# Performance work log

Measured on AMD Instinct MI355X. Metric: run time of the kernel, lower is better.

## Reference

```python
import jax, jax.numpy as jnp
import numpy as np

B, L, H = 8, 4096, 768  # batch, max_length, attn_size (hidden)


def setup_inputs() -> dict:
    key = jax.random.key(0)
    ks = jax.random.split(key, 8)
    s = 1.0 / np.sqrt(H)  # nn.Linear default init scale (uniform bound)
    x = jax.random.normal(ks[0], (B, L, H), dtype=jnp.float32)
    Wq = jax.random.uniform(ks[1], (H, H), jnp.float32, -s, s)
    bq = jax.random.uniform(ks[2], (H,), jnp.float32, -s, s)
    Wk = jax.random.uniform(ks[3], (H, H), jnp.float32, -s, s)
    bk = jax.random.uniform(ks[4], (H,), jnp.float32, -s, s)
    Wv = jax.random.uniform(ks[5], (H, H), jnp.float32, -s, s)
    bv = jax.random.uniform(ks[6], (H,), jnp.float32, -s, s)
    gamma = jnp.zeros((1,), dtype=jnp.float32)  # nn.Parameter(torch.zeros(1))
    return {"x": x, "Wq": Wq, "bq": bq, "Wk": Wk, "bk": bk,
            "Wv": Wv, "bv": bv, "gamma": gamma}


def reference(x, Wq, bq, Wk, bk, Wv, bv, gamma):
    # Linear projections: y = x @ W^T + b   (torch nn.Linear convention)
    q = jnp.einsum('bld,ed->ble', x, Wq) + bq  # (B, L, H)
    k = jnp.einsum('bld,ed->ble', x, Wk) + bk
    v = jnp.einsum('bld,ed->ble', x, Wv) + bv
    # energy = bmm(Q^T, K): contracts over sequence -> (B, H, H)
    energy = jnp.einsum('bld,ble->bde', q, k)
    attention = jax.nn.softmax(energy, axis=-1)  # (B, H, H), softmax over last hidden dim
    # out = bmm(V, attention^T): out[b,l,i] = sum_j V[b,l,j] * A[b,i,j]
    out = jnp.einsum('blj,bij->bli', v, attention)
    # neg_out uses (1 - A); since sum_j V[b,l,j]*(1-A[b,i,j]) = rowsum(V) - out,
    # we fuse instead of materializing a second bmm over (1 - A).
    neg_out = jnp.sum(v, axis=-1, keepdims=True) - out
    g = gamma[0]
    return (g * out + x, g * neg_out + x)
```

## Files before the change

kernel.cpp:

```cpp
#include <hip/hip_runtime.h>
#include <hip/hip_bf16.h>


#define HD 768
#define LSEQ 4096
#define BATCH 8
#define LDSS 40

typedef unsigned short u16;
typedef __attribute__((ext_vector_type(8))) short frag_ab;
typedef __attribute__((ext_vector_type(4))) float f32x4;

struct alignas(8) U16x4 { u16 x, y, z, w; };

__device__ inline u16 f2bf(float f) {
  union { float f; unsigned u; } v; v.f = f;
  unsigned u = v.u;
  u += 0x7FFFu + ((u >> 16) & 1u);
  return (u16)(u >> 16);
}


template <typename T>
__device__ inline void stage_tile(u16* lds, const T* src, int ld, int tid) {
#pragma unroll
  for (int i = 0; i < 4; ++i) {
    int idx = tid + 256 * i;
    int r = idx >> 3;
    int kv = (idx & 7) * 4;
    if constexpr (sizeof(T) == 4) {
      float4 v = *(const float4*)(src + (size_t)r * ld + kv);
      U16x4 h;
      h.x = f2bf(v.x); h.y = f2bf(v.y); h.z = f2bf(v.z); h.w = f2bf(v.w);
      *(U16x4*)(lds + r * LDSS + kv) = h;
    } else {
      *(U16x4*)(lds + r * LDSS + kv) = *(const U16x4*)(src + (size_t)r * ld + kv);
    }
  }
}

template <typename TP, typename TQ>
__device__ inline void gemm_core(const TP* Pt, const TQ* Qt, int ldp, int ldq, int K,
                                 u16* ldsA, u16* ldsB, f32x4 (&acc)[4][4]) {
  const int tid = threadIdx.x;
  const int lane = tid & 63;
  const int wm = tid >> 7, wn = (tid >> 6) & 1;
  for (int kk = 0; kk < K; kk += 32) {
    stage_tile(ldsA, Pt + kk, ldp, tid);
    stage_tile(ldsB, Qt + kk, ldq, tid);
    __syncthreads();
    const u16* bA = ldsA + (wm * 64 + (lane & 15)) * LDSS + 8 * (lane >> 4);
    const u16* bB = ldsB + (wn * 64 + (lane & 15)) * LDSS + 8 * (lane >> 4);
    frag_ab a[4], b[4];
#pragma unroll
    for (int i = 0; i < 4; ++i) a[i] = *(const frag_ab*)(bA + i * 16 * LDSS);
#pragma unroll
    for (int j = 0; j < 4; ++j) b[j] = *(const frag_ab*)(bB + j * 16 * LDSS);
#pragma unroll
    for (int i = 0; i < 4; ++i)
#pragma unroll
      for (int j = 0; j < 4; ++j)
        acc[i][j] = __builtin_amdgcn_mfma_f32_16x16x32_bf16(a[i], b[j], acc[i][j], 0, 0, 0);
    __syncthreads();
  }
}

template <typename TP, typename TQ>
__global__ __launch_bounds__(256) void k_gemm(const TP* __restrict__ P, const TQ* __restrict__ Q,
                                              float* __restrict__ C, int ldp, int ldq, int ldc,
                                              int K, int tilesM, int tilesN, long sP, long sQ,
                                              long sC) {
  __shared__ u16 ldsA[128 * LDSS];
  __shared__ u16 ldsB[128 * LDSS];
  int bid = blockIdx.x;
  int tn = bid % tilesN;
  int tm = (bid / tilesN) % tilesM;
  int b = bid / (tilesN * tilesM);
  const TP* Pt = P + b * sP + (long)(tm * 128) * ldp;
  const TQ* Qt = Q + b * sQ + (long)(tn * 128) * ldq;
  f32x4 acc[4][4] = {};
  gemm_core(Pt, Qt, ldp, ldq, K, ldsA, ldsB, acc);
  const int lane = threadIdx.x & 63;
  const int wm = threadIdx.x >> 7, wn = (threadIdx.x >> 6) & 1;
  float* Cb = C + b * sC;
#pragma unroll
  for (int i = 0; i < 4; ++i)
#pragma unroll
    for (int j = 0; j < 4; ++j)
#pragma unroll
      for (int r = 0; r < 4; ++r) {
        int row = tm * 128 + wm * 64 + i * 16 + 4 * (lane >> 4) + r;
        int col = tn * 128 + wn * 64 + j * 16 + (lane & 15);
        Cb[(long)row * ldc + col] = acc[i][j][r];
      }
}

__global__ __launch_bounds__(256) void k_gemm_bias(const float* __restrict__ P,
                                                   const float* __restrict__ Q,
                                                   float* __restrict__ C, long sP, long sC,
                                                   const float* __restrict__ bq,
                                                   const float* __restrict__ bk,
                                                   const float* __restrict__ qb,
                                                   const float* __restrict__ kbp) {
  __shared__ u16 ldsA[128 * LDSS];
  __shared__ u16 ldsB[128 * LDSS];
  int bid = blockIdx.x;
  int tn = bid % 6;
  int tm = (bid / 6) % 6;
  int b = bid / 36;
  const float* Pt = P + b * sP + (long)(tm * 128) * HD;
  const float* Qt = Q + (long)(tn * 128) * HD;
  f32x4 acc[4][4] = {};
  gemm_core(Pt, Qt, HD, HD, HD, ldsA, ldsB, acc);
  const int lane = threadIdx.x & 63;
  const int wm = threadIdx.x >> 7, wn = (threadIdx.x >> 6) & 1;
  float* Cb = C + b * sC;
  const float* qbb = qb + b * HD;
  const float* kbb = kbp + b * HD;
#pragma unroll
  for (int i = 0; i < 4; ++i)
#pragma unroll
    for (int j = 0; j < 4; ++j)
#pragma unroll
      for (int r = 0; r < 4; ++r) {
        int row = tm * 128 + wm * 64 + i * 16 + 4 * (lane >> 4) + r;
        int col = tn * 128 + wn * 64 + j * 16 + (lane & 15);
        Cb[(long)row * HD + col] = acc[i][j][r] + bq[row] * kbb[col] + bk[col] * qbb[row];
      }
}

__global__ __launch_bounds__(256) void k_final(const float* __restrict__ x,
                                               const float* __restrict__ Mw,
                                               const float* __restrict__ cvec,
                                               const float* __restrict__ rsv,
                                               const float* __restrict__ bvs,
                                               const float* __restrict__ gamma,
                                               float* __restrict__ out) {
  __shared__ u16 ldsA[128 * LDSS];
  __shared__ u16 ldsB[128 * LDSS];
  int bid = blockIdx.x;
  int tn = bid % 6;
  int tm = (bid / 6) % 32;
  int b = bid / 192;
  const float* Pt = x + ((long)b * LSEQ + tm * 128) * HD;
  const float* Qt = Mw + (long)b * HD * HD + (long)(tn * 128) * HD;
  f32x4 acc[4][4] = {};
  gemm_core(Pt, Qt, HD, HD, HD, ldsA, ldsB, acc);
  const int lane = threadIdx.x & 63;
  const int wm = threadIdx.x >> 7, wn = (threadIdx.x >> 6) & 1;
  const float g = gamma[0];
  const float bvsum = bvs[0];
  const float* cb = cvec + b * HD;
  const float* rb = rsv + b * LSEQ;
  float* out2 = out + (long)BATCH * LSEQ * HD;
#pragma unroll
  for (int i = 0; i < 4; ++i)
#pragma unroll
    for (int j = 0; j < 4; ++j)
#pragma unroll
      for (int r = 0; r < 4; ++r) {
        int row = tm * 128 + wm * 64 + i * 16 + 4 * (lane >> 4) + r;
        int col = tn * 128 + wn * 64 + j * 16 + (lane & 15);
        float o = acc[i][j][r] + cb[col];
        long gi = ((long)b * LSEQ + row) * HD + col;
        float xv = x[gi];
        out[gi] = g * o + xv;
        out2[gi] = g * ((rb[row] + bvsum) - o) + xv;
      }
}


__global__ __launch_bounds__(256) void k_trans(const float* __restrict__ x, u16* __restrict__ Xt,
                                               float* __restrict__ s, float* __restrict__ rsv,
                                               const float* __restrict__ wvsum) {
  __shared__ float tile[64][65];
  __shared__ float red[4][64];
  int bid = blockIdx.x;
  int ft = bid % 12;
  int lt = (bid / 12) % 64;
  int b = bid / 768;
  int l0 = lt * 64, f0 = ft * 64;
  const float* xb = x + ((long)b * LSEQ + l0) * HD + f0;
  int t = threadIdx.x;
  int fi = t & 63, tg = t >> 6;
  float csum = 0.f;
#pragma unroll
  for (int i = 0; i < 16; ++i) {
    int li = tg * 16 + i;
    float v = xb[(long)li * HD + fi];
    tile[li][fi] = v;
    csum += v;
  }
  red[tg][fi] = csum;
  __syncthreads();
  if (tg == 0) atomicAdd(&s[b * HD + f0 + fi], red[0][fi] + red[1][fi] + red[2][fi] + red[3][fi]);
  int li2 = t & 63, fg = t >> 6;
  float rsum = 0.f;
  u16* Xtb = Xt + ((long)b * HD + f0) * LSEQ + l0;
#pragma unroll
  for (int i = 0; i < 16; ++i) {
    int fi2 = fg * 16 + i;
    float v = tile[li2][fi2];
    rsum += v * wvsum[f0 + fi2];
    Xtb[(long)fi2 * LSEQ + li2] = f2bf(v);
  }
  __syncthreads();
  red[fg][li2] = rsum;
  __syncthreads();
  if (fg == 0)
    atomicAdd(&rsv[b * LSEQ + l0 + li2], red[0][li2] + red[1][li2] + red[2][li2] + red[3][li2]);
}

__global__ __launch_bounds__(256) void k_wv(const float* __restrict__ Wv, u16* __restrict__ WvT,
                                            float* __restrict__ wvsum) {
  __shared__ float red[256];
  long idx = (long)blockIdx.x * 256 + threadIdx.x;
  int f = (int)(idx / HD);
  int j = (int)(idx % HD);
  float v = Wv[(long)j * HD + f];
  WvT[(long)f * HD + j] = f2bf(v);
  red[threadIdx.x] = v;
  __syncthreads();
  for (int off = 128; off > 0; off >>= 1) {
    if (threadIdx.x < off) red[threadIdx.x] += red[threadIdx.x + off];
    __syncthreads();
  }
  if (threadIdx.x == 0) atomicAdd(&wvsum[f], red[0]);
}

__global__ __launch_bounds__(256) void k_bvsum(const float* __restrict__ bv,
                                               float* __restrict__ bvs) {
  __shared__ float red[256];
  int t = threadIdx.x;
  red[t] = bv[t] + bv[t + 256] + bv[t + 512];
  __syncthreads();
  for (int off = 128; off > 0; off >>= 1) {
    if (t < off) red[t] += red[t + off];
    __syncthreads();
  }
  if (t == 0) bvs[0] = red[0];
}

__global__ __launch_bounds__(256) void k_qbkb(const float* __restrict__ Wq,
                                              const float* __restrict__ Wk,
                                              const float* __restrict__ bk,
                                              const float* __restrict__ s, float* __restrict__ qb,
                                              float* __restrict__ kbp) {
  __shared__ float ss[HD];
  int idx = blockIdx.x * 256 + threadIdx.x;
  int b = idx / (2 * HD);
  int rem = idx % (2 * HD);
  int mat = rem / HD;
  int d = rem % HD;
  const float* sb = s + b * HD;
  ss[threadIdx.x] = sb[threadIdx.x];
  ss[threadIdx.x + 256] = sb[threadIdx.x + 256];
  ss[threadIdx.x + 512] = sb[threadIdx.x + 512];
  __syncthreads();
  const float* Wr = (mat ? Wk : Wq) + (long)d * HD;
  float acc = 0.f;
  for (int f2 = 0; f2 < HD; ++f2) acc += ss[f2] * Wr[f2];
  if (mat)
    kbp[b * HD + d] = acc + (float)LSEQ * bk[d];
  else
    qb[b * HD + d] = acc;
}

__device__ inline float block_red(float v, int op, float* sm) {
#pragma unroll
  for (int o = 32; o > 0; o >>= 1) {
    float w = __shfl_xor(v, o);
    v = op ? (v + w) : fmaxf(v, w);
  }
  int wid = threadIdx.x >> 6;
  if ((threadIdx.x & 63) == 0) sm[wid] = v;
  __syncthreads();
  float r = op ? (sm[0] + sm[1] + sm[2] + sm[3])
              : fmaxf(fmaxf(sm[0], sm[1]), fmaxf(sm[2], sm[3]));
  __syncthreads();
  return r;
}

__global__ __launch_bounds__(256) void k_softmax(float* __restrict__ A,
                                                 const float* __restrict__ bv,
                                                 float* __restrict__ cvec) {
  __shared__ float sm[4];
  long ridx = blockIdx.x;
  float* Ar = A + ridx * HD;
  int t = threadIdx.x;
  float v0 = Ar[t], v1 = Ar[t + 256], v2 = Ar[t + 512];
  float mx = block_red(fmaxf(fmaxf(v0, v1), v2), 0, sm);
  v0 = __expf(v0 - mx);
  v1 = __expf(v1 - mx);
  v2 = __expf(v2 - mx);
  float sum = block_red(v0 + v1 + v2, 1, sm);
  float inv = 1.0f / sum;
  v0 *= inv; v1 *= inv; v2 *= inv;
  Ar[t] = v0; Ar[t + 256] = v1; Ar[t + 512] = v2;
  float cp = v0 * bv[t] + v1 * bv[t + 256] + v2 * bv[t + 512];
  cp = block_red(cp, 1, sm);
  if (t == 0) cvec[ridx] = cp;
}

extern "C" void kernel_launch(void* const* d_in, const int* in_sizes, int n_in, void* d_out,
                              int out_size, void* d_ws, size_t ws_size, hipStream_t stream) {
  const float* x = (const float*)d_in[0];
  const float* Wq = (const float*)d_in[1];
  const float* bq = (const float*)d_in[2];
  const float* Wk = (const float*)d_in[3];
  const float* bk = (const float*)d_in[4];
  const float* Wv = (const float*)d_in[5];
  const float* bv = (const float*)d_in[6];
  const float* gamma = (const float*)d_in[7];
  float* out = (float*)d_out;

  float* ws = (float*)d_ws;
  float* s = ws;
  float* rsv = s + BATCH * HD;
  float* wvsum = rsv + BATCH * LSEQ;
  float* bvs = wvsum + HD;
  float* qb = bvs + 4;
  float* kbp = qb + BATCH * HD;
  float* cvec = kbp + BATCH * HD;
  u16* WvT = (u16*)(cvec + BATCH * HD);
  float* Mw = (float*)(WvT + HD * HD);

  u16* Xt = (u16*)d_out;
  float* G = (float*)d_out + 12582912;
  float* V1 = G + (long)BATCH * HD * HD;
  float* Abuf = V1 + (long)BATCH * HD * HD;

  size_t zbytes = (size_t)(BATCH * HD + BATCH * LSEQ + HD + 4) * sizeof(float);
  hipMemsetAsync(d_ws, 0, zbytes, stream);

  k_wv<<<2304, 256, 0, stream>>>(Wv, WvT, wvsum);
  k_bvsum<<<1, 256, 0, stream>>>(bv, bvs);
  k_trans<<<BATCH * 64 * 12, 256, 0, stream>>>(x, Xt, s, rsv, wvsum);
  k_gemm<u16, u16><<<BATCH * 36, 256, 0, stream>>>(Xt, Xt, G, LSEQ, LSEQ, HD, LSEQ, 6, 6,
                                                   (long)HD * LSEQ, (long)HD * LSEQ,
                                                   (long)HD * HD);
  k_qbkb<<<48, 256, 0, stream>>>(Wq, Wk, bk, s, qb, kbp);
  k_gemm<float, float><<<BATCH * 36, 256, 0, stream>>>(Wq, G, V1, HD, HD, HD, HD, 6, 6, 0L,
                                                       (long)HD * HD, (long)HD * HD);
  k_gemm_bias<<<BATCH * 36, 256, 0, stream>>>(V1, Wk, Abuf, (long)HD * HD, (long)HD * HD, bq, bk,
                                              qb, kbp);
  k_softmax<<<BATCH * HD, 256, 0, stream>>>(Abuf, bv, cvec);
  k_gemm<float, u16><<<BATCH * 36, 256, 0, stream>>>(Abuf, WvT, Mw, HD, HD, HD, HD, 6, 6,
                                                     (long)HD * HD, 0L, (long)HD * HD);
  k_final<<<BATCH * 32 * 6, 256, 0, stream>>>(x, Mw, cvec, rsv, bvs, gamma, out);
}
```

Before: 729.1 us.

## Stage bf16 intermediates and use direct global-to-LDS loads in GEMMs

Converts intermediate matrices (Gram, V1, attention, Mw) and the weights Wq/Wk to bf16 up front, so every GEMM operand except fp32 inputs is staged with async global_load_lds instead of per-thread load-convert-store. When workspace allows, the transpose kernel also writes a bf16 copy of x so the final GEMM reads half the bytes. LDS padding is dropped to fit the direct-load layout, which may introduce bank conflicts. The qb/kb dot product is also vectorised.

```diff
diff --git a/kernel.cpp b/kernel.cpp
--- a/kernel.cpp
+++ b/kernel.cpp
@@ -5,11 +5,12 @@
 #define HD 768
 #define LSEQ 4096
 #define BATCH 8
-#define LDSS 40
 
 typedef unsigned short u16;
 typedef __attribute__((ext_vector_type(8))) short frag_ab;
 typedef __attribute__((ext_vector_type(4))) float f32x4;
+#define AS1 __attribute__((address_space(1)))
+#define AS3 __attribute__((address_space(3)))
 
 struct alignas(8) U16x4 { u16 x, y, z, w; };
 
@@ -21,41 +22,51 @@
 }
 
 
-template <typename T>
-__device__ inline void stage_tile(u16* lds, const T* src, int ld, int tid) {
+__device__ inline void stage_g2l(u16* lds, const u16* src, int ld, int tid) {
+  int w = tid >> 6, l = tid & 63;
+  int r0 = w * 32 + (l >> 2);
+  int kc = (l & 3) * 8;
+  const u16* g0 = src + (size_t)r0 * ld + kc;
+  const u16* g1 = g0 + (size_t)16 * ld;
+  u16* l0 = lds + w * 1024;
+  u16* l1 = lds + w * 1024 + 512;
+  __builtin_amdgcn_global_load_lds((const AS1 void*)g0, (AS3 void*)l0, 16, 0, 0);
+  __builtin_amdgcn_global_load_lds((const AS1 void*)g1, (AS3 void*)l1, 16, 0, 0);
+}
+
+__device__ inline void stage_cvt(u16* lds, const float* src, int ld, int tid) {
 #pragma unroll
   for (int i = 0; i < 4; ++i) {
     int idx = tid + 256 * i;
     int r = idx >> 3;
     int kv = (idx & 7) * 4;
-    if constexpr (sizeof(T) == 4) {
-      float4 v = *(const float4*)(src + (size_t)r * ld + kv);
-      U16x4 h;
-      h.x = f2bf(v.x); h.y = f2bf(v.y); h.z = f2bf(v.z); h.w = f2bf(v.w);
-      *(U16x4*)(lds + r * LDSS + kv) = h;
-    } else {
-      *(U16x4*)(lds + r * LDSS + kv) = *(const U16x4*)(src + (size_t)r * ld + kv);
-    }
-  }
-}
-
-template <typename TP, typename TQ>
-__device__ inline void gemm_core(const TP* Pt, const TQ* Qt, int ldp, int ldq, int K,
+    float4 v = *(const float4*)(src + (size_t)r * ld + kv);
+    U16x4 h;
+    h.x = f2bf(v.x); h.y = f2bf(v.y); h.z = f2bf(v.z); h.w = f2bf(v.w);
+    *(U16x4*)(lds + r * 32 + kv) = h;
+  }
+}
+
+template <typename TP>
+__device__ inline void gemm_core(const TP* Pt, const u16* Qt, int ldp, int ldq, int K,
                                  u16* ldsA, u16* ldsB, f32x4 (&acc)[4][4]) {
   const int tid = threadIdx.x;
   const int lane = tid & 63;
   const int wm = tid >> 7, wn = (tid >> 6) & 1;
   for (int kk = 0; kk < K; kk += 32) {
-    stage_tile(ldsA, Pt + kk, ldp, tid);
-    stage_tile(ldsB, Qt + kk, ldq, tid);
+    if constexpr (sizeof(TP) == 2)
+      stage_g2l(ldsA, (const u16*)Pt + kk, ldp, tid);
+    else
+      stage_cvt(ldsA, (const float*)Pt + kk, ldp, tid);
+    stage_g2l(ldsB, Qt + kk, ldq, tid);
     __syncthreads();
-    const u16* bA = ldsA + (wm * 64 + (lane & 15)) * LDSS + 8 * (lane >> 4);
-    const u16* bB = ldsB + (wn * 64 + (lane & 15)) * LDSS + 8 * (lane >> 4);
+    const u16* bA = ldsA + (wm * 64 + (lane & 15)) * 32 + 8 * (lane >> 4);
+    const u16* bB = ldsB + (wn * 64 + (lane & 15)) * 32 + 8 * (lane >> 4);
     frag_ab a[4], b[4];
 #pragma unroll
-    for (int i = 0; i < 4; ++i) a[i] = *(const frag_ab*)(bA + i * 16 * LDSS);
-#pragma unroll
-    for (int j = 0; j < 4; ++j) b[j] = *(const frag_ab*)(bB + j * 16 * LDSS);
+    for (int i = 0; i < 4; ++i) a[i] = *(const frag_ab*)(bA + i * 16 * 32);
+#pragma unroll
+    for (int j = 0; j < 4; ++j) b[j] = *(const frag_ab*)(bB + j * 16 * 32);
 #pragma unroll
     for (int i = 0; i < 4; ++i)
 #pragma unroll
@@ -65,24 +76,24 @@
   }
 }
 
-template <typename TP, typename TQ>
-__global__ __launch_bounds__(256) void k_gemm(const TP* __restrict__ P, const TQ* __restrict__ Q,
-                                              float* __restrict__ C, int ldp, int ldq, int ldc,
-                                              int K, int tilesM, int tilesN, long sP, long sQ,
-                                              long sC) {
-  __shared__ u16 ldsA[128 * LDSS];
-  __shared__ u16 ldsB[128 * LDSS];
+template <typename CT>
+__global__ __launch_bounds__(256) void k_gemm_c(const u16* __restrict__ P,
+                                                const u16* __restrict__ Q, CT* __restrict__ C,
+                                                int ldp, int ldq, int ldc, int K, int tilesM,
+                                                int tilesN, long sP, long sQ, long sC) {
+  __shared__ u16 ldsA[128 * 32];
+  __shared__ u16 ldsB[128 * 32];
   int bid = blockIdx.x;
   int tn = bid % tilesN;
   int tm = (bid / tilesN) % tilesM;
   int b = bid / (tilesN * tilesM);
-  const TP* Pt = P + b * sP + (long)(tm * 128) * ldp;
-  const TQ* Qt = Q + b * sQ + (long)(tn * 128) * ldq;
+  const u16* Pt = P + b * sP + (long)(tm * 128) * ldp;
+  const u16* Qt = Q + b * sQ + (long)(tn * 128) * ldq;
   f32x4 acc[4][4] = {};
   gemm_core(Pt, Qt, ldp, ldq, K, ldsA, ldsB, acc);
   const int lane = threadIdx.x & 63;
   const int wm = threadIdx.x >> 7, wn = (threadIdx.x >> 6) & 1;
-  float* Cb = C + b * sC;
+  CT* Cb = C + b * sC;
 #pragma unroll
   for (int i = 0; i < 4; ++i)
 #pragma unroll
@@ -91,25 +102,28 @@
       for (int r = 0; r < 4; ++r) {
         int row = tm * 128 + wm * 64 + i * 16 + 4 * (lane >> 4) + r;
         int col = tn * 128 + wn * 64 + j * 16 + (lane & 15);
-        Cb[(long)row * ldc + col] = acc[i][j][r];
+        if constexpr (sizeof(CT) == 2)
+          Cb[(long)row * ldc + col] = f2bf(acc[i][j][r]);
+        else
+          Cb[(long)row * ldc + col] = acc[i][j][r];
       }
 }
 
-__global__ __launch_bounds__(256) void k_gemm_bias(const float* __restrict__ P,
-                                                   const float* __restrict__ Q,
+__global__ __launch_bounds__(256) void k_gemm_bias(const u16* __restrict__ P,
+                                                   const u16* __restrict__ Q,
                                                    float* __restrict__ C, long sP, long sC,
                                                    const float* __restrict__ bq,
                                                    const float* __restrict__ bk,
                                                    const float* __restrict__ qb,
                                                    const float* __restrict__ kbp) {
-  __shared__ u16 ldsA[128 * LDSS];
-  __shared__ u16 ldsB[128 * LDSS];
+  __shared__ u16 ldsA[128 * 32];
+  __shared__ u16 ldsB[128 * 32];
   int bid = blockIdx.x;
   int tn = bid % 6;
   int tm = (bid / 6) % 6;
   int b = bid / 36;
-  const float* Pt = P + b * sP + (long)(tm * 128) * HD;
-  const float* Qt = Q + (long)(tn * 128) * HD;
+  const u16* Pt = P + b * sP + (long)(tm * 128) * HD;
+  const u16* Qt = Q + (long)(tn * 128) * HD;
   f32x4 acc[4][4] = {};
   gemm_core(Pt, Qt, HD, HD, HD, ldsA, ldsB, acc);
   const int lane = threadIdx.x & 63;
@@ -129,21 +143,23 @@
       }
 }
 
-__global__ __launch_bounds__(256) void k_final(const float* __restrict__ x,
-                                               const float* __restrict__ Mw,
+template <typename TP>
+__global__ __launch_bounds__(256) void k_final(const TP* __restrict__ XP,
+                                               const float* __restrict__ x,
+                                               const u16* __restrict__ Mw,
                                                const float* __restrict__ cvec,
                                                const float* __restrict__ rsv,
                                                const float* __restrict__ bvs,
                                                const float* __restrict__ gamma,
                                                float* __restrict__ out) {
-  __shared__ u16 ldsA[128 * LDSS];
-  __shared__ u16 ldsB[128 * LDSS];
+  __shared__ u16 ldsA[128 * 32];
+  __shared__ u16 ldsB[128 * 32];
   int bid = blockIdx.x;
   int tn = bid % 6;
   int tm = (bid / 6) % 32;
   int b = bid / 192;
-  const float* Pt = x + ((long)b * LSEQ + tm * 128) * HD;
-  const float* Qt = Mw + (long)b * HD * HD + (long)(tn * 128) * HD;
+  const TP* Pt = XP + ((long)b * LSEQ + tm * 128) * HD;
+  const u16* Qt = Mw + (long)b * HD * HD + (long)(tn * 128) * HD;
   f32x4 acc[4][4] = {};
   gemm_core(Pt, Qt, HD, HD, HD, ldsA, ldsB, acc);
   const int lane = threadIdx.x & 63;
@@ -170,8 +186,10 @@
 }
 
 
+template <int WX>
 __global__ __launch_bounds__(256) void k_trans(const float* __restrict__ x, u16* __restrict__ Xt,
-                                               float* __restrict__ s, float* __restrict__ rsv,
+                                               u16* __restrict__ Xbf, float* __restrict__ s,
+                                               float* __restrict__ rsv,
                                                const float* __restrict__ wvsum) {
   __shared__ float tile[64][65];
   __shared__ float red[4][64];
@@ -190,6 +208,7 @@
     float v = xb[(long)li * HD + fi];
     tile[li][fi] = v;
     csum += v;
+    if constexpr (WX) Xbf[((long)b * LSEQ + l0 + li) * HD + f0 + fi] = f2bf(v);
   }
   red[tg][fi] = csum;
   __syncthreads();
@@ -226,6 +245,16 @@
     __syncthreads();
   }
   if (threadIdx.x == 0) atomicAdd(&wvsum[f], red[0]);
+}
+
+__global__ __launch_bounds__(256) void k_cvtw(const float* __restrict__ Wq,
+                                              const float* __restrict__ Wk,
+                                              u16* __restrict__ Wqh, u16* __restrict__ Wkh) {
+  int idx = blockIdx.x * 256 + threadIdx.x;
+  if (idx < HD * HD)
+    Wqh[idx] = f2bf(Wq[idx]);
+  else
+    Wkh[idx - HD * HD] = f2bf(Wk[idx - HD * HD]);
 }
 
 __global__ __launch_bounds__(256) void k_bvsum(const float* __restrict__ bv,
@@ -259,7 +288,10 @@
   __syncthreads();
   const float* Wr = (mat ? Wk : Wq) + (long)d * HD;
   float acc = 0.f;
-  for (int f2 = 0; f2 < HD; ++f2) acc += ss[f2] * Wr[f2];
+  for (int f2 = 0; f2 < HD; f2 += 4) {
+    float4 w4 = *(const float4*)(Wr + f2);
+    acc += ss[f2] * w4.x + ss[f2 + 1] * w4.y + ss[f2 + 2] * w4.z + ss[f2 + 3] * w4.w;
+  }
   if (mat)
     kbp[b * HD + d] = acc + (float)LSEQ * bk[d];
   else
@@ -281,14 +313,14 @@
   return r;
 }
 
-__global__ __launch_bounds__(256) void k_softmax(float* __restrict__ A,
+__global__ __launch_bounds__(256) void k_softmax(const float* __restrict__ E,
                                                  const float* __restrict__ bv,
-                                                 float* __restrict__ cvec) {
+                                                 u16* __restrict__ Ah, float* __restrict__ cvec) {
   __shared__ float sm[4];
   long ridx = blockIdx.x;
-  float* Ar = A + ridx * HD;
+  const float* Er = E + ridx * HD;
   int t = threadIdx.x;
-  float v0 = Ar[t], v1 = Ar[t + 256], v2 = Ar[t + 512];
+  float v0 = Er[t], v1 = Er[t + 256], v2 = Er[t + 512];
   float mx = block_red(fmaxf(fmaxf(v0, v1), v2), 0, sm);
   v0 = __expf(v0 - mx);
   v1 = __expf(v1 - mx);
@@ -296,7 +328,8 @@
   float sum = block_red(v0 + v1 + v2, 1, sm);
   float inv = 1.0f / sum;
   v0 *= inv; v1 *= inv; v2 *= inv;
-  Ar[t] = v0; Ar[t + 256] = v1; Ar[t + 512] = v2;
+  u16* Ar = Ah + ridx * HD;
+  Ar[t] = f2bf(v0); Ar[t + 256] = f2bf(v1); Ar[t + 512] = f2bf(v2);
   float cp = v0 * bv[t] + v1 * bv[t + 256] + v2 * bv[t + 512];
   cp = block_red(cp, 1, sm);
   if (t == 0) cvec[ridx] = cp;
@@ -319,33 +352,45 @@
   float* rsv = s + BATCH * HD;
   float* wvsum = rsv + BATCH * LSEQ;
   float* bvs = wvsum + HD;
-  float* qb = bvs + 4;
+  float* qb = bvs + 8;
   float* kbp = qb + BATCH * HD;
   float* cvec = kbp + BATCH * HD;
-  u16* WvT = (u16*)(cvec + BATCH * HD);
-  float* Mw = (float*)(WvT + HD * HD);
+  u16* Mh = (u16*)(cvec + BATCH * HD);
+  u16* Xbf = (u16*)((float*)Mh + 2359296);
+  size_t ws_need = (size_t)(6144 + 32768 + 768 + 8 + 3 * 6144 + 2359296 + 12582912) * 4;
+  bool fast = ws_size >= ws_need;
 
   u16* Xt = (u16*)d_out;
-  float* G = (float*)d_out + 12582912;
-  float* V1 = G + (long)BATCH * HD * HD;
-  float* Abuf = V1 + (long)BATCH * HD * HD;
-
-  size_t zbytes = (size_t)(BATCH * HD + BATCH * LSEQ + HD + 4) * sizeof(float);
+  float* Abuf = (float*)d_out + 12582912;
+  u16* Gh = (u16*)((float*)d_out + 17301504);
+  u16* V1h = (u16*)((float*)d_out + 19660800);
+  u16* Ah = (u16*)((float*)d_out + 22020096);
+  u16* WvT = (u16*)((float*)d_out + 24379392);
+  u16* Wqh = (u16*)((float*)d_out + 24674304);
+  u16* Wkh = (u16*)((float*)d_out + 24969216);
+
+  size_t zbytes = (size_t)(6144 + 32768 + 768 + 8) * sizeof(float);
   hipMemsetAsync(d_ws, 0, zbytes, stream);
 
+  k_cvtw<<<4608, 256, 0, stream>>>(Wq, Wk, Wqh, Wkh);
   k_wv<<<2304, 256, 0, stream>>>(Wv, WvT, wvsum);
   k_bvsum<<<1, 256, 0, stream>>>(bv, bvs);
-  k_trans<<<BATCH * 64 * 12, 256, 0, stream>>>(x, Xt, s, rsv, wvsum);
-  k_gemm<u16, u16><<<BATCH * 36, 256, 0, stream>>>(Xt, Xt, G, LSEQ, LSEQ, HD, LSEQ, 6, 6,
-                                                   (long)HD * LSEQ, (long)HD * LSEQ,
-                                                   (long)HD * HD);
+  if (fast)
+    k_trans<1><<<BATCH * 64 * 12, 256, 0, stream>>>(x, Xt, Xbf, s, rsv, wvsum);
+  else
+    k_trans<0><<<BATCH * 64 * 12, 256, 0, stream>>>(x, Xt, nullptr, s, rsv, wvsum);
+  k_gemm_c<u16><<<BATCH * 36, 256, 0, stream>>>(Xt, Xt, Gh, LSEQ, LSEQ, HD, LSEQ, 6, 6,
+                                                (long)HD * LSEQ, (long)HD * LSEQ, (long)HD * HD);
   k_qbkb<<<48, 256, 0, stream>>>(Wq, Wk, bk, s, qb, kbp);
-  k_gemm<float, float><<<BATCH * 36, 256, 0, stream>>>(Wq, G, V1, HD, HD, HD, HD, 6, 6, 0L,
-                                                       (long)HD * HD, (long)HD * HD);
-  k_gemm_bias<<<BATCH * 36, 256, 0, stream>>>(V1, Wk, Abuf, (long)HD * HD, (long)HD * HD, bq, bk,
-                                              qb, kbp);
-  k_softmax<<<BATCH * HD, 256, 0, stream>>>(Abuf, bv, cvec);
-  k_gemm<float, u16><<<BATCH * 36, 256, 0, stream>>>(Abuf, WvT, Mw, HD, HD, HD, HD, 6, 6,
-                                                     (long)HD * HD, 0L, (long)HD * HD);
-  k_final<<<BATCH * 32 * 6, 256, 0, stream>>>(x, Mw, cvec, rsv, bvs, gamma, out);
-}
+  k_gemm_c<u16><<<BATCH * 36, 256, 0, stream>>>(Wqh, Gh, V1h, HD, HD, HD, HD, 6, 6, 0L,
+                                                (long)HD * HD, (long)HD * HD);
+  k_gemm_bias<<<BATCH * 36, 256, 0, stream>>>(V1h, Wkh, Abuf, (long)HD * HD, (long)HD * HD, bq,
+                                              bk, qb, kbp);
+  k_softmax<<<BATCH * HD, 256, 0, stream>>>(Abuf, bv, Ah, cvec);
+  k_gemm_c<u16><<<BATCH * 36, 256, 0, stream>>>(Ah, WvT, Mh, HD, HD, HD, HD, 6, 6,
+                                                (long)HD * HD, 0L, (long)HD * HD);
+  if (fast)
+    k_final<u16><<<BATCH * 32 * 6, 256, 0, stream>>>(Xbf, x, Mh, cvec, rsv, bvs, gamma, out);
+  else
+    k_final<float><<<BATCH * 32 * 6, 256, 0, stream>>>(x, x, Mh, cvec, rsv, bvs, gamma, out);
+}
```

New measurement: 665.5 us. -8.7%, faster.
